# Kernel tuning notes

Hardware: AMD Instinct MI355X
Metric: run time of the kernel (lower is better)

The kernel has to match this reference:

```python
import jax, jax.numpy as jnp
import numpy as np

ALPHA = 1.702
LIMIT = 7.0
BLOCK = 32  # mxfp4 block size (values per scale)

# fp4 e2m1 lookup table, indexed by 4-bit code (sign in high bit)
FP4_LUT = jnp.array([0.0, 0.5, 1.0, 1.5, 2.0, 3.0, 4.0, 6.0,
                     -0.0, -0.5, -1.0, -1.5, -2.0, -3.0, -4.0, -6.0],
                    dtype=jnp.float32)


def dequant_mxfp4(blocks, scales):
    # blocks: [E, R, C//2] int byte values (two fp4 nibbles per byte, low nibble first)
    # scales: [E, R, C//32] e8m0 exponents; value = 2^(scale - 127)
    E, R, _ = blocks.shape
    nb = scales.shape[-1]
    lo = blocks & 0xF
    hi = (blocks >> 4) & 0xF
    vals = jnp.stack([FP4_LUT[lo], FP4_LUT[hi]], axis=-1)  # [E,R,C//2,2]
    vals = vals.reshape(E, R, nb, BLOCK)
    scale = jnp.exp2((scales - 127).astype(jnp.float32))   # [E,R,nb]
    return (vals * scale[..., None]).reshape(E, R, nb * BLOCK)  # [E,R,C]


def setup_inputs() -> dict:
    key = jax.random.key(0)
    ks = jax.random.split(key, 12)
    T, E, H, I = 1024, 8, 1024, 1024
    inp = {
        'hidden_states': jax.random.normal(ks[0], (T, H), dtype=jnp.float32),
        'router_logits': jax.random.normal(ks[1], (T, E), dtype=jnp.float32),
        'gate_proj_blocks': jax.random.randint(ks[2], (E, I, H // 2), 0, 256, dtype=jnp.int32),
        'gate_proj_scales': jax.random.randint(ks[3], (E, I, H // BLOCK), 121, 130, dtype=jnp.int32),
        'gate_proj_bias': jax.random.normal(ks[4], (E, I), dtype=jnp.float32) * 0.02,
        'up_proj_blocks': jax.random.randint(ks[5], (E, I, H // 2), 0, 256, dtype=jnp.int32),
        'up_proj_scales': jax.random.randint(ks[6], (E, I, H // BLOCK), 121, 130, dtype=jnp.int32),
        'up_proj_bias': jax.random.normal(ks[7], (E, I), dtype=jnp.float32) * 0.02,
        'down_proj_blocks': jax.random.randint(ks[8], (E, H, I // 2), 0, 256, dtype=jnp.int32),
        'down_proj_scales': jax.random.randint(ks[9], (E, H, I // BLOCK), 121, 130, dtype=jnp.int32),
        'down_proj_bias': jax.random.normal(ks[10], (E, H), dtype=jnp.float32) * 0.02,
        'k': 2,
    }
    return inp


def reference(hidden_states, router_logits, gate_proj_blocks, gate_proj_scales,
              gate_proj_bias, up_proj_blocks, up_proj_scales, up_proj_bias,
              down_proj_blocks, down_proj_scales, down_proj_bias, k):
    T, H = hidden_states.shape
    E = router_logits.shape[-1]
    # --- top-k routing: softmax over the selected logits, scattered to [T,E] ---
    top_vals, top_idx = jax.lax.top_k(router_logits, k)        # [T,k]
    top_w = jax.nn.softmax(top_vals, axis=-1)                   # [T,k]
    route = jnp.zeros((T, E), dtype=hidden_states.dtype)
    route = route.at[jnp.arange(T)[:, None], top_idx].add(top_w)  # [T,E]
    # --- dequantize mxfp4 expert weights ---
    gate_w = dequant_mxfp4(gate_proj_blocks, gate_proj_scales)  # [E,I,H]
    up_w = dequant_mxfp4(up_proj_blocks, up_proj_scales)        # [E,I,H]
    down_w = dequant_mxfp4(down_proj_blocks, down_proj_scales)  # [E,H,I]
    # --- GLU expert FFN (GPT-OSS variant) ---
    gate = jnp.einsum('th,eih->tei', hidden_states, gate_w) + gate_proj_bias[None]
    up = jnp.einsum('th,eih->tei', hidden_states, up_w) + up_proj_bias[None]
    gate = jnp.minimum(gate, LIMIT)
    up = jnp.clip(up, -LIMIT, LIMIT)
    glu = gate * jax.nn.sigmoid(gate * ALPHA)
    act = (up + 1.0) * glu                                       # [T,E,I]
    # fold routing weight in before the down projection, then sum over experts
    act = act * route[:, :, None]
    out = jnp.einsum('tei,ehi->th', act, down_w) + route @ down_proj_bias  # [T,H]
    return out
```

## Files before the change

kernel.cpp:

```cpp
#include <hip/hip_runtime.h>
#include <cstdint>
#include <cstddef>

typedef __bf16 bf16x8 __attribute__((ext_vector_type(8)));
typedef __bf16 bf16x2 __attribute__((ext_vector_type(2)));
typedef float f32x16 __attribute__((ext_vector_type(16)));
typedef unsigned short u16x2 __attribute__((ext_vector_type(2)));

constexpr int HH = 1024;
constexpr int II = 1024;
constexpr int KMAX = 2;
constexpr int EMAX = 8;
constexpr int GU_TILES = 24;
constexpr int DN_TILES = 40;
constexpr float FALPHA = 1.702f;
constexpr float FLIMIT = 7.0f;

#if __has_builtin(__builtin_amdgcn_cvt_scalef32_pk_bf16_fp4)
#define USE_CVT 1
#else
#define USE_CVT 0
#endif

#define SCHED0() __builtin_amdgcn_sched_barrier(0)

__device__ __forceinline__ unsigned pk_add16(unsigned a, unsigned b) {
  u16x2 x, y;
  __builtin_memcpy(&x, &a, 4); __builtin_memcpy(&y, &b, 4);
  u16x2 r = x + y;
  unsigned o; __builtin_memcpy(&o, &r, 4); return o;
}
__device__ __forceinline__ int4 decode_chunk(int4 raw, unsigned addk) {
  unsigned p = (unsigned)raw.x | ((unsigned)raw.y << 8) |
               ((unsigned)raw.z << 16) | ((unsigned)raw.w << 24);
  unsigned q = p >> 4;
  unsigned me = p & 0x07070707u, mo = q & 0x07070707u;
  unsigned se = p & 0x08080808u, so = q & 0x08080808u;
  unsigned hiE = __builtin_amdgcn_perm(0x40404040u, 0x3F3F3F14u, me) | (se << 4);
  unsigned hiO = __builtin_amdgcn_perm(0x40404040u, 0x3F3F3F14u, mo) | (so << 4);
  unsigned loE = __builtin_amdgcn_perm(0xC0804000u, 0xC0800000u, me);
  unsigned loO = __builtin_amdgcn_perm(0xC0804000u, 0xC0800000u, mo);
  int4 out;
  out.x = (int)pk_add16(__builtin_amdgcn_perm(hiE, loE, 0x05010400u), addk);
  out.y = (int)pk_add16(__builtin_amdgcn_perm(hiE, loE, 0x07030602u), addk);
  out.z = (int)pk_add16(__builtin_amdgcn_perm(hiO, loO, 0x05010400u), addk);
  out.w = (int)pk_add16(__builtin_amdgcn_perm(hiO, loO, 0x07030602u), addk);
  return out;
}
__device__ __forceinline__ unsigned make_addk(int s) {
  int k = s - 127;
  unsigned t = ((unsigned)(k << 7)) & 0xFFFFu;
  return t | (t << 16);
}

__device__ __forceinline__ bf16x8 decode_frag(int4 raw, int s) {
#if USE_CVT
  unsigned t0 = __builtin_amdgcn_perm((unsigned)raw.y, (unsigned)raw.x, 0x00000400u);
  unsigned t1 = __builtin_amdgcn_perm((unsigned)raw.w, (unsigned)raw.z, 0x00000400u);
  unsigned p  = __builtin_amdgcn_perm(t1, t0, 0x05040100u);
  float scf = __uint_as_float((unsigned)s << 23);
  bf16x2 a = __builtin_amdgcn_cvt_scalef32_pk_bf16_fp4(p, scf, 0);
  bf16x2 b = __builtin_amdgcn_cvt_scalef32_pk_bf16_fp4(p, scf, 1);
  bf16x2 c = __builtin_amdgcn_cvt_scalef32_pk_bf16_fp4(p, scf, 2);
  bf16x2 d = __builtin_amdgcn_cvt_scalef32_pk_bf16_fp4(p, scf, 3);
  bf16x8 r;
  r[0]=a[0]; r[1]=a[1]; r[2]=b[0]; r[3]=b[1]; r[4]=c[0]; r[5]=c[1]; r[6]=d[0]; r[7]=d[1];
  return r;
#else
  int4 d4 = decode_chunk(raw, make_addk(s));
  bf16x8 r; __builtin_memcpy(&r, &d4, 16);
  return r;
#endif
}

__device__ __forceinline__ void gll16(const void* g, void* l) {
  __builtin_amdgcn_global_load_lds(
      (const __attribute__((address_space(1))) void*)g,
      (__attribute__((address_space(3))) void*)l, 16, 0, 0);
}

__device__ __forceinline__ int xcd_swz(int wg, int nwg) {
  int q = nwg >> 3, r = nwg & 7;
  int xcd = wg & 7, pos = wg >> 3;
  return (xcd < r ? xcd * (q + 1) : r * (q + 1) + (xcd - r) * q) + pos;
}

__global__ __launch_bounds__(1024) void prep_convert(
    const float* __restrict__ logits, const int* __restrict__ dk, int T, int E,
    float* __restrict__ route, float* __restrict__ tw,
    int* __restrict__ lists, int* __restrict__ counts,
    int* __restrict__ tabGU, int* __restrict__ tabDN,
    const float* __restrict__ hs, __bf16* __restrict__ hsb, int n8) {
  if ((int)blockIdx.x < (int)gridDim.x - 1) {
    int g = blockIdx.x * 1024 + threadIdx.x;
    if (g < n8) {
      const float4* p = (const float4*)hs + (size_t)g * 2;
      float4 a = p[0], b = p[1];
      bf16x8 r;
#if USE_CVT
      r[0] = (__bf16)a.x; r[1] = (__bf16)a.y; r[2] = (__bf16)a.z; r[3] = (__bf16)a.w;
      r[4] = (__bf16)b.x; r[5] = (__bf16)b.y; r[6] = (__bf16)b.z; r[7] = (__bf16)b.w;
#else
      r[0] = (__bf16)a.x; r[1] = (__bf16)a.z; r[2] = (__bf16)b.x; r[3] = (__bf16)b.z;
      r[4] = (__bf16)a.y; r[5] = (__bf16)a.w; r[6] = (__bf16)b.y; r[7] = (__bf16)b.w;
#endif
      *(bf16x8*)(hsb + (size_t)g * 8) = r;
    }
    return;
  }
  __shared__ unsigned char s_ti[1024];
  __shared__ int s_cnt[EMAX];
  int t = threadIdx.x;
  int kk = *dk; if (kk > KMAX) kk = KMAX; if (kk < 1) kk = 1;
  int EE = E > EMAX ? EMAX : E;
  if (t < T) {
    float v[EMAX]; bool used[EMAX];
    for (int e = 0; e < EE; ++e) { v[e] = logits[t * E + e]; used[e] = false; route[t * E + e] = 0.f; }
    float tv[KMAX]; int ti[KMAX];
    for (int j = 0; j < kk; ++j) {
      float best = -3.4e38f; int bi = 0;
      for (int e = 0; e < EE; ++e) if (!used[e] && v[e] > best) { best = v[e]; bi = e; }
      used[bi] = true; tv[j] = best; ti[j] = bi;
    }
    float mx = tv[0], ssum = 0.f, wj[KMAX];
    for (int j = 0; j < kk; ++j) { wj[j] = __expf(tv[j] - mx); ssum += wj[j]; }
    for (int j = 0; j < kk; ++j) {
      float wv = wj[j] / ssum;
      route[t * E + ti[j]] = wv;
      tw[t * kk + j] = wv;
    }
    s_ti[t] = (unsigned char)(ti[0] | ((kk > 1 ? ti[1] : 0xF) << 4));
  } else if (t < 1024) {
    s_ti[t] = 0xFF;
  }
  __syncthreads();
  int w = t >> 6, lane = t & 63;
  if (w < EE) {
    int e = w, cnt = 0;
    for (int base = 0; base < T; base += 64) {
      int tt = base + lane;
      int j = -1;
      if (tt < T) {
        int packed = s_ti[tt];
        if ((packed & 0xF) == e) j = 0;
        else if ((packed >> 4) == e) j = 1;
      }
      unsigned long long m = __ballot(j >= 0);
      if (j >= 0) {
        int pre = __popcll(m & ((1ull << lane) - 1ull));
        lists[e * T + cnt + pre] = (tt << 3) | j;
      }
      cnt += __popcll(m);
    }
    if (lane == 0) { counts[e] = cnt; s_cnt[e] = cnt; }
  }
  __syncthreads();
  if (t == 0) {
    int g = 0, d = 0;
    for (int e = 0; e < EE; ++e) {
      int c = s_cnt[e];
      for (int m = 0; m * 128 < c && g < GU_TILES; ++m) tabGU[g++] = (e << 16) | m;
      for (int m = 0; m * 64 < c && d < DN_TILES; ++m) tabDN[d++] = (e << 16) | m;
    }
    for (; g < GU_TILES; ++g) tabGU[g] = -1;
    for (; d < DN_TILES; ++d) tabDN[d] = -1;
  }
}

__global__ __launch_bounds__(512, 2) void gemm_gate_up(
    const __bf16* __restrict__ hsb,
    const int* __restrict__ gblk, const int* __restrict__ gscl, const float* __restrict__ gbias,
    const int* __restrict__ ublk, const int* __restrict__ uscl, const float* __restrict__ ubias,
    const int* __restrict__ lists, const int* __restrict__ counts,
    const float* __restrict__ tw, const int* __restrict__ dk,
    const int* __restrict__ tab,
    __bf16* __restrict__ act, int T)
{
  int lin = xcd_swz(blockIdx.x, GU_TILES * (II / 64));
  int ntile = lin / GU_TILES, xt = lin % GU_TILES;
  int te = tab[xt];
  if (te < 0) return;
  int e = te >> 16, mtile = te & 0xFFFF;
  int cnt = counts[e];
  int n_valid = cnt - mtile * 128;
  if (n_valid <= 0) return;
  if (n_valid > 128) n_valid = 128;
  int kk = *dk; if (kk > KMAX) kk = KMAX; if (kk < 1) kk = 1;
  int ibase = ntile * 64;

  __shared__ int s_tok[128];
  __shared__ __attribute__((aligned(16))) char Abuf[2][16384];
  __shared__ __attribute__((aligned(16))) char Bbuf[2][16384];
  __shared__ __attribute__((aligned(8))) unsigned short sS[128][36];

  int tid = threadIdx.x;
  if (tid < 128) {
    int idx = mtile * 128 + tid;
    s_tok[tid] = lists[e * T + (idx < cnt ? idx : mtile * 128)];
  }
  __syncthreads();

  int lane = tid & 63, w = tid >> 6;
  int wr = w >> 2, wc = w & 3;
  int l31 = lane & 31, kg2 = lane >> 5;
  int sub = lane >> 3, cL = lane & 7;
  int cA = cL ^ (sub & 7);

  const char* aSrc[2];
  #pragma unroll
  for (int q = 0; q < 2; ++q) {
    int row = w * 16 + q * 8 + sub;
    int tok = s_tok[row] >> 3;
    aSrc[q] = (const char*)hsb + (size_t)tok * (HH * 2) + (size_t)cA * 16;
  }
  const char* bSrc[2];
  #pragma unroll
  for (int q = 0; q < 2; ++q) {
    int row = w * 16 + q * 8 + sub;
    int mat = (row >> 4) & 1;
    int i = ibase + ((row >> 5) << 4) + (row & 15);
    const int* base = mat ? ublk : gblk;
    bSrc[q] = (const char*)(base + ((size_t)e * II + i) * (HH / 2)) + (size_t)cA * 16;
  }

  int4 sv4[2];
  #pragma unroll
  for (int rep = 0; rep < 2; ++rep) {
    int idx = tid + rep * 512;
    int row = idx >> 3, c4 = idx & 7;
    int mat = (row >> 4) & 1;
    int i = ibase + ((row >> 5) << 4) + (row & 15);
    const int* sbase = mat ? uscl : gscl;
    sv4[rep] = *((const int4*)(sbase + ((size_t)e * II + i) * 32) + c4);
  }
  asm volatile("s_waitcnt vmcnt(0)" ::: "memory");
  SCHED0();
  #pragma unroll
  for (int rep = 0; rep < 2; ++rep) {
    int idx = tid + rep * 512;
    int row = idx >> 3, c4 = idx & 7;
    unsigned short* dst = &sS[row][c4 * 4];
    dst[0] = (unsigned short)sv4[rep].x; dst[1] = (unsigned short)sv4[rep].y;
    dst[2] = (unsigned short)sv4[rep].z; dst[3] = (unsigned short)sv4[rep].w;
  }
  #pragma unroll
  for (int q = 0; q < 2; ++q) {
    gll16(aSrc[q], Abuf[0] + (w * 16 + q * 8) * 128);
    gll16(bSrc[q], Bbuf[0] + (w * 16 + q * 8) * 128);
  }
  #pragma unroll
  for (int q = 0; q < 2; ++q) {
    gll16(aSrc[q] + 128, Abuf[1] + (w * 16 + q * 8) * 128);
    gll16(bSrc[q] + 128, Bbuf[1] + (w * 16 + q * 8) * 128);
  }
  asm volatile("s_waitcnt vmcnt(4)" ::: "memory");
  asm volatile("s_waitcnt lgkmcnt(0)" ::: "memory");
  SCHED0();
  __builtin_amdgcn_s_barrier();
  SCHED0();

  f32x16 acc0 = (f32x16)0.f, acc1 = (f32x16)0.f;
  int brow = wc * 32 + l31;

  constexpr int NK = HH / 64;
  #pragma unroll 1
  for (int t = 0; t < NK; ++t) {
    const char* Ac = Abuf[t & 1];
    const char* Bc = Bbuf[t & 1];
    unsigned sv = *(const unsigned*)((const char*)sS + brow * 72 + t * 4);
    #pragma unroll
    for (int s = 0; s < 4; ++s) {
      int kc = kg2 + 2 * s;
      int4 rawb = *(const int4*)(Bc + brow * 128 + ((kc ^ (brow & 7)) << 4));
      bf16x8 bb = decode_frag(rawb, (s >> 1) ? (int)(sv >> 16) : (int)(sv & 0xFFFF));
      int m0 = wr * 64 + l31;
      bf16x8 a0 = *(const bf16x8*)(Ac + m0 * 128 + ((kc ^ (m0 & 7)) << 4));
      int m1 = m0 + 32;
      bf16x8 a1 = *(const bf16x8*)(Ac + m1 * 128 + ((kc ^ (m1 & 7)) << 4));
      acc0 = __builtin_amdgcn_mfma_f32_32x32x16_bf16(a0, bb, acc0, 0, 0, 0);
      acc1 = __builtin_amdgcn_mfma_f32_32x32x16_bf16(a1, bb, acc1, 0, 0, 0);
    }
    asm volatile("s_waitcnt lgkmcnt(0)" ::: "memory");
    SCHED0();
    __builtin_amdgcn_s_barrier();
    SCHED0();
    if (t + 2 < NK) {
      char* An = Abuf[t & 1];
      char* Bn = Bbuf[t & 1];
      #pragma unroll
      for (int q = 0; q < 2; ++q) {
        gll16(aSrc[q] + (t + 2) * 128, An + (w * 16 + q * 8) * 128);
        gll16(bSrc[q] + (t + 2) * 128, Bn + (w * 16 + q * 8) * 128);
      }
      asm volatile("s_waitcnt vmcnt(4)" ::: "memory");
    } else {
      asm volatile("s_waitcnt vmcnt(0)" ::: "memory");
    }
    SCHED0();
    __builtin_amdgcn_s_barrier();
    SCHED0();
  }

  {
    bool isGate = (l31 & 16) == 0;
    int i_log = ibase + wc * 16 + (l31 & 15);
    float gb = gbias[e * II + i_log], ub = ubias[e * II + i_log];
#if USE_CVT
    int i_st = i_log;
#else
    int i_st = (i_log & ~7) | ((i_log & 1) << 2) | ((i_log & 7) >> 1);
#endif
    #pragma unroll
    for (int r = 0; r < 16; ++r) {
      float gv = acc0[r];
      float ov = __shfl_xor(gv, 16);
      int row = wr * 64 + (r & 3) + 8 * (r >> 2) + 4 * kg2;
      if (isGate && row < n_valid) {
        int entry = s_tok[row];
        int t2 = entry >> 3, j = entry & 7;
        float wv = tw[t2 * kk + j];
        float g = fminf(gv + gb, FLIMIT);
        float u = fminf(fmaxf(ov + ub, -FLIMIT), FLIMIT);
        float glu = g / (1.f + __expf(-FALPHA * g));
        act[((size_t)t2 * kk + j) * II + i_st] = (__bf16)((u + 1.f) * glu * wv);
      }
    }
    #pragma unroll
    for (int r = 0; r < 16; ++r) {
      float gv = acc1[r];
      float ov = __shfl_xor(gv, 16);
      int row = wr * 64 + (r & 3) + 8 * (r >> 2) + 4 * kg2 + 32;
      if (isGate && row < n_valid) {
        int entry = s_tok[row];
        int t2 = entry >> 3, j = entry & 7;
        float wv = tw[t2 * kk + j];
        float g = fminf(gv + gb, FLIMIT);
        float u = fminf(fmaxf(ov + ub, -FLIMIT), FLIMIT);
        float glu = g / (1.f + __expf(-FALPHA * g));
        act[((size_t)t2 * kk + j) * II + i_st] = (__bf16)((u + 1.f) * glu * wv);
      }
    }
  }
}

__global__ __launch_bounds__(512, 2) void gemm_down(
    const __bf16* __restrict__ act,
    const int* __restrict__ dblk, const int* __restrict__ dscl,
    const int* __restrict__ lists, const int* __restrict__ counts,
    const int* __restrict__ dk, const int* __restrict__ tab,
    __bf16* __restrict__ partial, int T)
{
  int lin = xcd_swz(blockIdx.x, DN_TILES * (HH / 128));
  int ntile = lin / DN_TILES, xt = lin % DN_TILES;
  int te = tab[xt];
  if (te < 0) return;
  int e = te >> 16, mtile = te & 0xFFFF;
  int cnt = counts[e];
  int n_valid = cnt - mtile * 64;
  if (n_valid <= 0) return;
  if (n_valid > 64) n_valid = 64;
  int kk = *dk; if (kk > KMAX) kk = KMAX; if (kk < 1) kk = 1;
  int hbase = ntile * 128;

  __shared__ int s_tok[64];
  __shared__ __attribute__((aligned(16))) char Abuf[2][8192];
  __shared__ __attribute__((aligned(16))) char Bbuf[2][16384];
  __shared__ __attribute__((aligned(8))) unsigned short sS[128][36];

  int tid = threadIdx.x;
  if (tid < 64) {
    int idx = mtile * 64 + tid;
    s_tok[tid] = lists[e * T + (idx < cnt ? idx : mtile * 64)];
  }
  __syncthreads();

  int lane = tid & 63, w = tid >> 6;
  int wr = w >> 2, wc = w & 3;
  int l31 = lane & 31, kg2 = lane >> 5;
  int sub = lane >> 3, cL = lane & 7;
  int cA = cL ^ (sub & 7);

  const char* aSrc0;
  {
    int row = w * 8 + sub;
    int entry = s_tok[row];
    size_t slot = (size_t)(entry >> 3) * kk + (entry & 7);
    aSrc0 = (const char*)act + slot * (II * 2) + (size_t)cA * 16;
  }
  const char* bSrc[2];
  #pragma unroll
  for (int q = 0; q < 2; ++q) {
    int row = w * 16 + q * 8 + sub;
    bSrc[q] = (const char*)(dblk + ((size_t)e * HH + hbase + row) * (II / 2)) + (size_t)cA * 16;
  }

  int4 sv4[2];
  #pragma unroll
  for (int rep = 0; rep < 2; ++rep) {
    int idx = tid + rep * 512;
    int row = idx >> 3, c4 = idx & 7;
    sv4[rep] = *((const int4*)(dscl + ((size_t)e * HH + hbase + row) * 32) + c4);
  }
  asm volatile("s_waitcnt vmcnt(0)" ::: "memory");
  SCHED0();
  #pragma unroll
  for (int rep = 0; rep < 2; ++rep) {
    int idx = tid + rep * 512;
    int row = idx >> 3, c4 = idx & 7;
    unsigned short* dst = &sS[row][c4 * 4];
    dst[0] = (unsigned short)sv4[rep].x; dst[1] = (unsigned short)sv4[rep].y;
    dst[2] = (unsigned short)sv4[rep].z; dst[3] = (unsigned short)sv4[rep].w;
  }
  {
    gll16(aSrc0, Abuf[0] + (w * 8) * 128);
    #pragma unroll
    for (int q = 0; q < 2; ++q) gll16(bSrc[q], Bbuf[0] + (w * 16 + q * 8) * 128);
    gll16(aSrc0 + 128, Abuf[1] + (w * 8) * 128);
    #pragma unroll
    for (int q = 0; q < 2; ++q) gll16(bSrc[q] + 128, Bbuf[1] + (w * 16 + q * 8) * 128);
  }
  asm volatile("s_waitcnt vmcnt(3)" ::: "memory");
  asm volatile("s_waitcnt lgkmcnt(0)" ::: "memory");
  SCHED0();
  __builtin_amdgcn_s_barrier();
  SCHED0();

  f32x16 acc0 = (f32x16)0.f;
  int brow = wc * 32 + l31;
  int m0 = wr * 32 + l31;

  constexpr int NK = II / 64;
  #pragma unroll 1
  for (int t = 0; t < NK; ++t) {
    const char* Ac = Abuf[t & 1];
    const char* Bc = Bbuf[t & 1];
    unsigned sv = *(const unsigned*)((const char*)sS + brow * 72 + t * 4);
    #pragma unroll
    for (int s = 0; s < 4; ++s) {
      int kc = kg2 + 2 * s;
      int4 rawb = *(const int4*)(Bc + brow * 128 + ((kc ^ (brow & 7)) << 4));
      bf16x8 bb = decode_frag(rawb, (s >> 1) ? (int)(sv >> 16) : (int)(sv & 0xFFFF));
      bf16x8 a0 = *(const bf16x8*)(Ac + m0 * 128 + ((kc ^ (m0 & 7)) << 4));
      acc0 = __builtin_amdgcn_mfma_f32_32x32x16_bf16(a0, bb, acc0, 0, 0, 0);
    }
    asm volatile("s_waitcnt lgkmcnt(0)" ::: "memory");
    SCHED0();
    __builtin_amdgcn_s_barrier();
    SCHED0();
    if (t + 2 < NK) {
      char* An = Abuf[t & 1];
      char* Bn = Bbuf[t & 1];
      gll16(aSrc0 + (t + 2) * 128, An + (w * 8) * 128);
      #pragma unroll
      for (int q = 0; q < 2; ++q)
        gll16(bSrc[q] + (t + 2) * 128, Bn + (w * 16 + q * 8) * 128);
      asm volatile("s_waitcnt vmcnt(3)" ::: "memory");
    } else {
      asm volatile("s_waitcnt vmcnt(0)" ::: "memory");
    }
    SCHED0();
    __builtin_amdgcn_s_barrier();
    SCHED0();
  }

  {
    int h = hbase + wc * 32 + l31;
    #pragma unroll
    for (int r = 0; r < 16; ++r) {
      int row = wr * 32 + (r & 3) + 8 * (r >> 2) + 4 * kg2;
      if (row < n_valid) {
        int entry = s_tok[row];
        int t2 = entry >> 3, j = entry & 7;
        partial[((size_t)t2 * kk + j) * HH + h] = (__bf16)acc0[r];
      }
    }
  }
}

__global__ void combine_kernel(const __bf16* __restrict__ partial, const float* __restrict__ route,
                               const float* __restrict__ dbias, const int* __restrict__ dk,
                               float* __restrict__ out, int E) {
  int t = blockIdx.y;
  int h = blockIdx.x * 256 + threadIdx.x;
  int kk = *dk; if (kk > KMAX) kk = KMAX; if (kk < 1) kk = 1;
  float s = 0.f;
  for (int j = 0; j < kk; ++j) s += (float)partial[((size_t)t * kk + j) * HH + h];
  for (int e = 0; e < E; ++e) s += route[t * E + e] * dbias[(size_t)e * HH + h];
  out[(size_t)t * HH + h] = s;
}

extern "C" void kernel_launch(void* const* d_in, const int* in_sizes, int n_in,
                              void* d_out, int out_size, void* d_ws, size_t ws_size,
                              hipStream_t stream) {
  const float* hs    = (const float*)d_in[0];
  const float* rl    = (const float*)d_in[1];
  const int*   gblk  = (const int*)d_in[2];
  const int*   gscl  = (const int*)d_in[3];
  const float* gbias = (const float*)d_in[4];
  const int*   ublk  = (const int*)d_in[5];
  const int*   uscl  = (const int*)d_in[6];
  const float* ubias = (const float*)d_in[7];
  const int*   dblk  = (const int*)d_in[8];
  const int*   dscl  = (const int*)d_in[9];
  const float* dbias = (const float*)d_in[10];
  const int*   dk    = (const int*)d_in[11];

  long s0 = in_sizes[0], s1 = in_sizes[1], s2 = in_sizes[2], s4 = in_sizes[4];
  int H = (int)(2 * s2 / s4);
  int T = (int)(s0 / H);
  int E = (int)(s1 / T);

  char* w = (char*)d_ws;
  auto alloc = [&](size_t bytes) { char* p = w; w += (bytes + 255) & ~size_t(255); return p; };
  float*  route   = (float*)alloc(sizeof(float) * (size_t)T * E);
  float*  twp     = (float*)alloc(sizeof(float) * (size_t)T * KMAX);
  int*    counts  = (int*)  alloc(sizeof(int)   * (size_t)E);
  int*    lists   = (int*)  alloc(sizeof(int)   * (size_t)E * T);
  int*    tabGU   = (int*)  alloc(sizeof(int)   * GU_TILES);
  int*    tabDN   = (int*)  alloc(sizeof(int)   * DN_TILES);
  __bf16* hsb     = (__bf16*)alloc(sizeof(__bf16) * (size_t)T * HH);
  __bf16* act     = (__bf16*)alloc(sizeof(__bf16) * (size_t)T * KMAX * II);
  __bf16* partial = (__bf16*)alloc(sizeof(__bf16) * (size_t)T * KMAX * HH);

  int n8 = T * HH / 8;
  int nConv = (n8 + 1023) / 1024;
  prep_convert<<<dim3(nConv + 1), 1024, 0, stream>>>(
      rl, dk, T, E, route, twp, lists, counts, tabGU, tabDN, hs, hsb, n8);
  gemm_gate_up<<<dim3(GU_TILES * (II / 64)), 512, 0, stream>>>(
      hsb, gblk, gscl, gbias, ublk, uscl, ubias, lists, counts, twp, dk, tabGU, act, T);
  gemm_down<<<dim3(DN_TILES * (HH / 128)), 512, 0, stream>>>(
      act, dblk, dscl, lists, counts, dk, tabDN, partial, T);
  combine_kernel<<<dim3(HH / 256, T), 256, 0, stream>>>(partial, route, dbias, dk, (float*)d_out, E);
}
```

Before: 96.22 us.

## Triple-buffer GEMM K-loop and rotate K start per block

Both the gate/up and down GEMM kernels move from a double-buffered to a triple-buffered LDS pipeline, keeping two K-slices of global loads in flight instead of one. Each block also starts its K loop at a rotated offset derived from its linear tile index, so concurrent blocks read different K columns of the shared activation and weight rows. The aim is to hide more memory latency and spread DRAM/L2 traffic across channels. In exchange LDS use grows by half, which may cut occupancy below the two blocks per CU the launch bounds request.

```diff
diff --git a/kernel.cpp b/kernel.cpp
--- a/kernel.cpp
+++ b/kernel.cpp
@@ -187,10 +187,11 @@
   if (n_valid > 128) n_valid = 128;
   int kk = *dk; if (kk > KMAX) kk = KMAX; if (kk < 1) kk = 1;
   int ibase = ntile * 64;
+  int koff = (lin * 5) & 15;
 
   __shared__ int s_tok[128];
-  __shared__ __attribute__((aligned(16))) char Abuf[2][16384];
-  __shared__ __attribute__((aligned(16))) char Bbuf[2][16384];
+  __shared__ __attribute__((aligned(16))) char Abuf[3][16384];
+  __shared__ __attribute__((aligned(16))) char Bbuf[3][16384];
   __shared__ __attribute__((aligned(8))) unsigned short sS[128][36];
 
   int tid = threadIdx.x;
@@ -244,16 +245,15 @@
     dst[2] = (unsigned short)sv4[rep].z; dst[3] = (unsigned short)sv4[rep].w;
   }
   #pragma unroll
-  for (int q = 0; q < 2; ++q) {
-    gll16(aSrc[q], Abuf[0] + (w * 16 + q * 8) * 128);
-    gll16(bSrc[q], Bbuf[0] + (w * 16 + q * 8) * 128);
-  }
-  #pragma unroll
-  for (int q = 0; q < 2; ++q) {
-    gll16(aSrc[q] + 128, Abuf[1] + (w * 16 + q * 8) * 128);
-    gll16(bSrc[q] + 128, Bbuf[1] + (w * 16 + q * 8) * 128);
-  }
-  asm volatile("s_waitcnt vmcnt(4)" ::: "memory");
+  for (int b = 0; b < 3; ++b) {
+    int ks = (b + koff) & 15;
+    #pragma unroll
+    for (int q = 0; q < 2; ++q) {
+      gll16(aSrc[q] + ks * 128, Abuf[b] + (w * 16 + q * 8) * 128);
+      gll16(bSrc[q] + ks * 128, Bbuf[b] + (w * 16 + q * 8) * 128);
+    }
+  }
+  asm volatile("s_waitcnt vmcnt(8)" ::: "memory");
   asm volatile("s_waitcnt lgkmcnt(0)" ::: "memory");
   SCHED0();
   __builtin_amdgcn_s_barrier();
@@ -265,9 +265,11 @@
   constexpr int NK = HH / 64;
   #pragma unroll 1
   for (int t = 0; t < NK; ++t) {
-    const char* Ac = Abuf[t & 1];
-    const char* Bc = Bbuf[t & 1];
-    unsigned sv = *(const unsigned*)((const char*)sS + brow * 72 + t * 4);
+    int bi = t % 3;
+    int ks = (t + koff) & 15;
+    const char* Ac = Abuf[bi];
+    const char* Bc = Bbuf[bi];
+    unsigned sv = *(const unsigned*)((const char*)sS + brow * 72 + ks * 4);
     #pragma unroll
     for (int s = 0; s < 4; ++s) {
       int kc = kg2 + 2 * s;
@@ -284,14 +286,15 @@
     SCHED0();
     __builtin_amdgcn_s_barrier();
     SCHED0();
-    if (t + 2 < NK) {
-      char* An = Abuf[t & 1];
-      char* Bn = Bbuf[t & 1];
+    if (t + 3 < NK) {
+      int ksn = (t + 3 + koff) & 15;
       #pragma unroll
       for (int q = 0; q < 2; ++q) {
-        gll16(aSrc[q] + (t + 2) * 128, An + (w * 16 + q * 8) * 128);
-        gll16(bSrc[q] + (t + 2) * 128, Bn + (w * 16 + q * 8) * 128);
+        gll16(aSrc[q] + ksn * 128, Abuf[bi] + (w * 16 + q * 8) * 128);
+        gll16(bSrc[q] + ksn * 128, Bbuf[bi] + (w * 16 + q * 8) * 128);
       }
+      asm volatile("s_waitcnt vmcnt(8)" ::: "memory");
+    } else if (t + 2 < NK) {
       asm volatile("s_waitcnt vmcnt(4)" ::: "memory");
     } else {
       asm volatile("s_waitcnt vmcnt(0)" ::: "memory");
@@ -361,10 +364,11 @@
   if (n_valid > 64) n_valid = 64;
   int kk = *dk; if (kk > KMAX) kk = KMAX; if (kk < 1) kk = 1;
   int hbase = ntile * 128;
+  int koff = (lin * 5) & 15;
 
   __shared__ int s_tok[64];
-  __shared__ __attribute__((aligned(16))) char Abuf[2][8192];
-  __shared__ __attribute__((aligned(16))) char Bbuf[2][16384];
+  __shared__ __attribute__((aligned(16))) char Abuf[3][8192];
+  __shared__ __attribute__((aligned(16))) char Bbuf[3][16384];
   __shared__ __attribute__((aligned(8))) unsigned short sS[128][36];
 
   int tid = threadIdx.x;
@@ -411,15 +415,15 @@
     dst[0] = (unsigned short)sv4[rep].x; dst[1] = (unsigned short)sv4[rep].y;
     dst[2] = (unsigned short)sv4[rep].z; dst[3] = (unsigned short)sv4[rep].w;
   }
-  {
-    gll16(aSrc0, Abuf[0] + (w * 8) * 128);
-    #pragma unroll
-    for (int q = 0; q < 2; ++q) gll16(bSrc[q], Bbuf[0] + (w * 16 + q * 8) * 128);
-    gll16(aSrc0 + 128, Abuf[1] + (w * 8) * 128);
-    #pragma unroll
-    for (int q = 0; q < 2; ++q) gll16(bSrc[q] + 128, Bbuf[1] + (w * 16 + q * 8) * 128);
-  }
-  asm volatile("s_waitcnt vmcnt(3)" ::: "memory");
+  #pragma unroll
+  for (int b = 0; b < 3; ++b) {
+    int ks = (b + koff) & 15;
+    gll16(aSrc0 + ks * 128, Abuf[b] + (w * 8) * 128);
+    #pragma unroll
+    for (int q = 0; q < 2; ++q)
+      gll16(bSrc[q] + ks * 128, Bbuf[b] + (w * 16 + q * 8) * 128);
+  }
+  asm volatile("s_waitcnt vmcnt(6)" ::: "memory");
   asm volatile("s_waitcnt lgkmcnt(0)" ::: "memory");
   SCHED0();
   __builtin_amdgcn_s_barrier();
@@ -432,9 +436,11 @@
   constexpr int NK = II / 64;
   #pragma unroll 1
   for (int t = 0; t < NK; ++t) {
-    const char* Ac = Abuf[t & 1];
-    const char* Bc = Bbuf[t & 1];
-    unsigned sv = *(const unsigned*)((const char*)sS + brow * 72 + t * 4);
+    int bi = t % 3;
+    int ks = (t + koff) & 15;
+    const char* Ac = Abuf[bi];
+    const char* Bc = Bbuf[bi];
+    unsigned sv = *(const unsigned*)((const char*)sS + brow * 72 + ks * 4);
     #pragma unroll
     for (int s = 0; s < 4; ++s) {
       int kc = kg2 + 2 * s;
@@ -447,13 +453,14 @@
     SCHED0();
     __builtin_amdgcn_s_barrier();
     SCHED0();
-    if (t + 2 < NK) {
-      char* An = Abuf[t & 1];
-      char* Bn = Bbuf[t & 1];
-      gll16(aSrc0 + (t + 2) * 128, An + (w * 8) * 128);
+    if (t + 3 < NK) {
+      int ksn = (t + 3 + koff) & 15;
+      gll16(aSrc0 + ksn * 128, Abuf[bi] + (w * 8) * 128);
       #pragma unroll
       for (int q = 0; q < 2; ++q)
-        gll16(bSrc[q] + (t + 2) * 128, Bn + (w * 16 + q * 8) * 128);
+        gll16(bSrc[q] + ksn * 128, Bbuf[bi] + (w * 16 + q * 8) * 128);
+      asm volatile("s_waitcnt vmcnt(6)" ::: "memory");
+    } else if (t + 2 < NK) {
       asm volatile("s_waitcnt vmcnt(3)" ::: "memory");
     } else {
       asm volatile("s_waitcnt vmcnt(0)" ::: "memory");
```

Result: slower. 130.6 us (+35.7%).
